# Kernel optimization log

Hardware: AMD Instinct MI355X
Metric: run time of the kernel (lower is better)

Reference implementation:

```python
import jax, jax.numpy as jnp
import numpy as np

DT = 0.01  # module-level constant in the original source
H = 64


def _lstm_cell(x_in, h, c, W_ih, W_hh, b_ih, b_hh):
    # torch nn.LSTM gate order: i, f, g, o
    gates = x_in @ W_ih.T + h @ W_hh.T + (b_ih + b_hh)
    i, f, g, o = jnp.split(gates, 4, axis=-1)
    i = jax.nn.sigmoid(i)
    f = jax.nn.sigmoid(f)
    g = jnp.tanh(g)
    o = jax.nn.sigmoid(o)
    c_new = f * c + i * g
    h_new = o * jnp.tanh(c_new)
    return h_new, c_new


def setup_inputs() -> dict:
    key = jax.random.key(0)
    ks = jax.random.split(key, 12)
    B, x_size, s_size = 4096, 8, 8
    in_size = x_size + s_size
    sc = 1.0 / np.sqrt(H)

    def rn(k, shape, scale=1.0):
        return (jax.random.normal(k, shape, dtype=jnp.float32) * scale)

    return {
        "x": rn(ks[0], (B, 1, x_size)),
        "s0": rn(ks[1], (B, s_size)),
        "W_ih0": rn(ks[2], (4 * H, in_size), sc),
        "W_hh0": rn(ks[3], (4 * H, H), sc),
        "b_ih0": rn(ks[4], (4 * H,), sc),
        "b_hh0": rn(ks[5], (4 * H,), sc),
        "W_ih1": rn(ks[6], (4 * H, H), sc),
        "W_hh1": rn(ks[7], (4 * H, H), sc),
        "b_ih1": rn(ks[8], (4 * H,), sc),
        "b_hh1": rn(ks[9], (4 * H,), sc),
        "fc_W": rn(ks[10], (s_size, H), sc),
        "fc_b": rn(ks[11], (s_size,), sc),
        "num_steps": 1001,  # floor(max_time/dt)+1 with max_time=10.0
    }


def reference(x, s0, W_ih0, W_hh0, b_ih0, b_hh0, W_ih1, W_hh1, b_ih1, b_hh1,
              fc_W, fc_b, num_steps):
    B = x.shape[0]
    xin = x[:, 0, :]  # forward only ever reads x[:, 0:1] -> [B, x_size]
    h0 = jnp.zeros((B, H), x.dtype)

    def step(carry, _):
        s, h_a, c_a, h_b, c_b = carry
        combined = jnp.concatenate([xin, s], axis=-1)  # [B, x_size + s_size]
        h_a, c_a = _lstm_cell(combined, h_a, c_a, W_ih0, W_hh0, b_ih0, b_hh0)
        h_b, c_b = _lstm_cell(h_a, h_b, c_b, W_ih1, W_hh1, b_ih1, b_hh1)
        step_out = h_b @ fc_W.T + fc_b            # [B, s_size]
        s_new = s + step_out * DT                  # Euler integration
        return (s_new, h_a, c_a, h_b, c_b), (s_new, step_out)

    init = (s0, h0, h0, h0, h0)
    _, (outs, res) = jax.lax.scan(step, init, None, length=num_steps)
    outputs = jnp.transpose(outs, (1, 0, 2))       # [B, num_steps, s_size]
    res_step = jnp.transpose(res, (1, 0, 2))       # [B, num_steps, s_size]
    cal_times = jnp.arange(num_steps, dtype=jnp.float32) * DT
    return outputs, cal_times, res_step
```

## Files before the change

### kernel.cpp

```cpp
#include <hip/hip_runtime.h>

#define DTC 0.01f
#define LAM  2.88539008178f
#define L2E  1.44269504089f

typedef __attribute__((ext_vector_type(8))) short short8;
typedef __attribute__((ext_vector_type(4))) float floatx4;

#if __has_builtin(__builtin_amdgcn_exp2f)
#define EXP2F(x) __builtin_amdgcn_exp2f(x)
#else
#define EXP2F(x) exp2f(x)
#endif
#if __has_builtin(__builtin_amdgcn_rcpf)
#define RCPF(x) __builtin_amdgcn_rcpf(x)
#else
#define RCPF(x) (1.0f / (x))
#endif

__device__ __forceinline__ unsigned short f2bf(float f) {
    unsigned u = __float_as_uint(f);
    u += 0x7FFFu + ((u >> 16) & 1u);
    return (unsigned short)(u >> 16);
}
__device__ __forceinline__ float rcp1p(float y) {
    return RCPF(1.0f + EXP2F(y));
}
__device__ __forceinline__ void wg_barrier() {
    asm volatile("s_waitcnt lgkmcnt(0)" ::: "memory");
    __builtin_amdgcn_s_barrier();
}
__device__ __forceinline__ float lane_merge(float lo, float hi) {
#if __has_builtin(__builtin_amdgcn_permlane32_swap)
    typedef __attribute__((ext_vector_type(2))) unsigned int uint2v;
    uint2v r = __builtin_amdgcn_permlane32_swap(__float_as_uint(lo), __float_as_uint(hi),
                                                false, false);
    return __uint_as_float(r[0]);
#else
    unsigned a = __float_as_uint(lo), b = __float_as_uint(hi);
    asm volatile("v_permlane32_swap_b32 %0, %1" : "+v"(a), "+v"(b));
    return __uint_as_float(a);
#endif
}

#define U1S 136

#define MFMA(a, b, c) __builtin_amdgcn_mfma_f32_16x16x32_bf16((a), (b), (c), 0, 0, 0)

__global__ __launch_bounds__(256, 2) void lstm_mfma(
    const float* __restrict__ x,    const float* __restrict__ s0,
    const float* __restrict__ W_ih0,const float* __restrict__ W_hh0,
    const float* __restrict__ b_ih0,const float* __restrict__ b_hh0,
    const float* __restrict__ W_ih1,const float* __restrict__ W_hh1,
    const float* __restrict__ b_ih1,const float* __restrict__ b_hh1,
    const float* __restrict__ fc_W, const float* __restrict__ fc_b,
    const int* __restrict__ nsp,    float* __restrict__ out, int B)
{
    __shared__ __align__(16) unsigned short U1[16 * U1S];

    const int ns   = nsp[0];
    const int tid  = threadIdx.x;
    const int lane = tid & 63;
    const int wave = tid >> 6;
    const int il   = lane & 15;
    const int quad = lane >> 4;
    const int bb   = blockIdx.x * 8;

    float* cal = out + (size_t)B * ns * 8;
    float* res = cal + ns;

    if (blockIdx.x == 0)
        for (int t = tid; t < ns; t += 256) cal[t] = t * DTC;

    for (int i = tid; i < 16 * U1S; i += 256) U1[i] = 0;

    short8 B0[4][2], B1[4][4], M2f[4][2], BF[2];
    floatx4 gs[4];
    float gd[4], b1s[4];

    for (int j = 0; j < 4; ++j) {
        const float gam = (j == 2) ? LAM : -L2E;
        const int n = 64 * j + 16 * wave + il;
        float ws[8];
        #pragma unroll
        for (int p = 0; p < 8; ++p) ws[p] = W_ih0[n * 16 + 8 + p];

        #pragma unroll
        for (int kk = 0; kk < 2; ++kk) {
            short8 f;
            #pragma unroll
            for (int jj = 0; jj < 8; ++jj) {
                int k = 32 * kk + 8 * quad + jj;
                f[jj] = (short)f2bf(gam * W_hh0[n * 64 + k]);
            }
            B0[j][kk] = f;
        }
        #pragma unroll
        for (int kk = 0; kk < 4; ++kk) {
            short8 f;
            #pragma unroll
            for (int jj = 0; jj < 8; ++jj) {
                int k = 32 * kk + 8 * quad + jj;
                float w = (k < 64) ? W_ih1[n * 64 + k] : W_hh1[n * 64 + (k - 64)];
                f[jj] = (short)f2bf(gam * w);
            }
            B1[j][kk] = f;
        }
        #pragma unroll
        for (int kk = 0; kk < 2; ++kk) {
            short8 f;
            #pragma unroll
            for (int jj = 0; jj < 8; ++jj) {
                int k = 32 * kk + 8 * quad + jj;
                float acc = 0.0f;
                #pragma unroll
                for (int p = 0; p < 8; ++p) acc += ws[p] * fc_W[p * 64 + k];
                f[jj] = (short)f2bf(gam * DTC * acc);
            }
            M2f[j][kk] = f;
        }
        float accb = 0.0f;
        #pragma unroll
        for (int p = 0; p < 8; ++p) accb += ws[p] * fc_b[p];
        gd[j] = gam * DTC * accb;

        float bcol = b_ih0[n] + b_hh0[n];
        floatx4 gv;
        #pragma unroll
        for (int reg = 0; reg < 4; ++reg) {
            int m  = 4 * quad + reg;
            int mr = bb + (m & 7);
            float acc = bcol;
            #pragma unroll
            for (int k = 0; k < 8; ++k) acc += x[mr * 8 + k] * W_ih0[n * 16 + k];
            #pragma unroll
            for (int p = 0; p < 8; ++p) acc += ws[p] * s0[mr * 8 + p];
            gv[reg] = gam * acc - gd[j];
        }
        gs[j] = gv;
        b1s[j] = gam * (b_ih1[n] + b_hh1[n]);
    }
    #pragma unroll
    for (int kk = 0; kk < 2; ++kk) {
        short8 f;
        #pragma unroll
        for (int jj = 0; jj < 8; ++jj) {
            int k = 32 * kk + 8 * quad + jj;
            float w = (il < 8) ? fc_W[il * 64 + k] : 0.0f;
            f[jj] = (short)f2bf(w);
        }
        BF[kk] = f;
    }
    const float fcb = (il < 8) ? fc_b[il] : 0.0f;

    const int mbase = 4 * ((lane & 31) >> 4) + ((lane >> 5) << 1);
    const int iidx  = 16 * wave + il;
    float cA[2] = {0, 0}, cB[2] = {0, 0};
    float s_reg[4];
    #pragma unroll
    for (int reg = 0; reg < 4; ++reg) {
        int m = 4 * quad + reg;
        s_reg[reg] = (il < 8 && m < 8) ? s0[(bb + m) * 8 + il] : 0.0f;
    }

    short8 a10 = {0,0,0,0,0,0,0,0};
    short8 a11 = {0,0,0,0,0,0,0,0};

    const unsigned short* Ar = &U1[il * U1S + 8 * quad];
    unsigned short* Hw = &U1[mbase * U1S + iidx];

    wg_barrier();

    #pragma unroll 1
    for (int t = 0; t < ns; ++t) {
        short8 a12 = *(const short8*)(Ar + 64);
        short8 a13 = *(const short8*)(Ar + 96);

        floatx4 q0[4], p1[4];
        #pragma unroll
        for (int j = 0; j < 4; ++j) {
            floatx4 z = gs[j];
            z = MFMA(a12, M2f[j][0], z);
            z = MFMA(a13, M2f[j][1], z);
            #pragma unroll
            for (int r = 0; r < 4; ++r) z[r] += gd[j];
            gs[j] = z;
            floatx4 q = z;
            q = MFMA(a10, B0[j][0], q);
            q = MFMA(a11, B0[j][1], q);
            q0[j] = q;
            floatx4 pz = {b1s[j], b1s[j], b1s[j], b1s[j]};
            pz = MFMA(a13, B1[j][3], pz);
            pz = MFMA(a12, B1[j][2], pz);
            p1[j] = pz;
        }
        float P[2][4];
        #pragma unroll
        for (int j = 0; j < 4; ++j) {
            P[0][j] = lane_merge(q0[j][0], q0[j][2]);
            P[1][j] = lane_merge(q0[j][1], q0[j][3]);
        }
        #pragma unroll
        for (int e = 0; e < 2; ++e) {
            float iv = rcp1p(P[e][0]);
            float fv = rcp1p(P[e][1]);
            float gr = rcp1p(P[e][2]);
            float ov = rcp1p(P[e][3]);
            float gl = __builtin_fmaf(gr, -2.0f * LAM, LAM);
            float c  = __builtin_fmaf(fv, cA[e], iv * gl);
            cA[e]    = c;
            float r2 = rcp1p(c);
            float h  = __builtin_fmaf(-2.0f, ov * r2, ov);
            Hw[e * U1S] = f2bf(h);
        }
        wg_barrier();

        a10 = *(const short8*)(Ar + 0);
        a11 = *(const short8*)(Ar + 32);

        if (t && wave == 0) {
            floatx4 so = {fcb, fcb, fcb, fcb};
            so = MFMA(a12, BF[0], so);
            so = MFMA(a13, BF[1], so);
            #pragma unroll
            for (int reg = 0; reg < 4; ++reg) {
                s_reg[reg] += so[reg] * DTC;
                if (quad < 2 && il < 8) {
                    size_t o = ((size_t)(bb + 4 * quad + reg) * ns + (t - 1)) * 8 + il;
                    out[o] = s_reg[reg];
                    res[o] = so[reg];
                }
            }
        }

        floatx4 q1[4];
        #pragma unroll
        for (int j = 0; j < 4; ++j) {
            floatx4 z = p1[j];
            z = MFMA(a10, B1[j][0], z);
            z = MFMA(a11, B1[j][1], z);
            q1[j] = z;
        }
        float Q[2][4];
        #pragma unroll
        for (int j = 0; j < 4; ++j) {
            Q[0][j] = lane_merge(q1[j][0], q1[j][2]);
            Q[1][j] = lane_merge(q1[j][1], q1[j][3]);
        }
        #pragma unroll
        for (int e = 0; e < 2; ++e) {
            float iv = rcp1p(Q[e][0]);
            float fv = rcp1p(Q[e][1]);
            float gr = rcp1p(Q[e][2]);
            float ov = rcp1p(Q[e][3]);
            float gl = __builtin_fmaf(gr, -2.0f * LAM, LAM);
            float c  = __builtin_fmaf(fv, cB[e], iv * gl);
            cB[e]    = c;
            float r2 = rcp1p(c);
            float h  = __builtin_fmaf(-2.0f, ov * r2, ov);
            Hw[e * U1S + 64] = f2bf(h);
        }
        wg_barrier();
    }

    if (wave == 0) {
        short8 a12 = *(const short8*)(Ar + 64);
        short8 a13 = *(const short8*)(Ar + 96);
        floatx4 so = {fcb, fcb, fcb, fcb};
        so = MFMA(a12, BF[0], so);
        so = MFMA(a13, BF[1], so);
        #pragma unroll
        for (int reg = 0; reg < 4; ++reg) {
            s_reg[reg] += so[reg] * DTC;
            if (quad < 2 && il < 8) {
                size_t o = ((size_t)(bb + 4 * quad + reg) * ns + (ns - 1)) * 8 + il;
                out[o] = s_reg[reg];
                res[o] = so[reg];
            }
        }
    }
}

extern "C" void kernel_launch(void* const* d_in, const int* in_sizes, int n_in,
                              void* d_out, int out_size, void* d_ws, size_t ws_size,
                              hipStream_t stream) {
    const float* x     = (const float*)d_in[0];
    const float* s0    = (const float*)d_in[1];
    const float* W_ih0 = (const float*)d_in[2];
    const float* W_hh0 = (const float*)d_in[3];
    const float* b_ih0 = (const float*)d_in[4];
    const float* b_hh0 = (const float*)d_in[5];
    const float* W_ih1 = (const float*)d_in[6];
    const float* W_hh1 = (const float*)d_in[7];
    const float* b_ih1 = (const float*)d_in[8];
    const float* b_hh1 = (const float*)d_in[9];
    const float* fc_W  = (const float*)d_in[10];
    const float* fc_b  = (const float*)d_in[11];
    const int*   nsp   = (const int*)d_in[12];
    (void)d_ws; (void)ws_size; (void)n_in; (void)out_size;
    int B = in_sizes[0] / 8;
    dim3 grid(B / 8), block(256);
    hipLaunchKernelGGL(lstm_mfma, grid, block, 0, stream,
        x, s0, W_ih0, W_hh0, b_ih0, b_hh0, W_ih1, W_hh1, b_ih1, b_hh1,
        fc_W, fc_b, nsp, (float*)d_out, B);
}
```

Measured before the change: 1.561 ms.

## Interleave two independent batch groups per block to overlap MFMA and transcendental phases

Each workgroup now handles 16 batch rows split into two independent 8-row groups with separate LDS buffers. The per-step schedule is software-pipelined so one group's MFMA phase runs alongside the other group's gate nonlinearities and state update, hiding the serial latency of the recurrence. Grid size is halved and launch bounds change to one block per SIMD set, which trades occupancy for more in-block parallelism and roughly doubles register pressure. The number of barriers per timestep also doubles.

```diff
diff --git a/kernel.cpp b/kernel.cpp
--- a/kernel.cpp
+++ b/kernel.cpp
@@ -47,7 +47,75 @@
 
 #define MFMA(a, b, c) __builtin_amdgcn_mfma_f32_16x16x32_bf16((a), (b), (c), 0, 0, 0)
 
-__global__ __launch_bounds__(256, 2) void lstm_mfma(
+__device__ __forceinline__ void mfma_phase1(
+    const short8& a0, const short8& a1, const short8& a2, const short8& a3,
+    const short8 B0[4][2], const short8 B1[4][4], const short8 M2f[4][2],
+    floatx4 gs[4], const float gd[4], const float b1s[4],
+    floatx4 q0[4], floatx4 p1[4])
+{
+    #pragma unroll
+    for (int j = 0; j < 4; ++j) {
+        floatx4 z = gs[j];
+        z = MFMA(a2, M2f[j][0], z);
+        z = MFMA(a3, M2f[j][1], z);
+        #pragma unroll
+        for (int r = 0; r < 4; ++r) z[r] += gd[j];
+        gs[j] = z;
+        floatx4 q = z;
+        q = MFMA(a0, B0[j][0], q);
+        q = MFMA(a1, B0[j][1], q);
+        q0[j] = q;
+        floatx4 pz = {b1s[j], b1s[j], b1s[j], b1s[j]};
+        pz = MFMA(a2, B1[j][2], pz);
+        pz = MFMA(a3, B1[j][3], pz);
+        p1[j] = pz;
+    }
+}
+
+__device__ __forceinline__ void cell_trans(const floatx4 q[4], float cst[2],
+                                           unsigned short* Hw)
+{
+    float P[2][4];
+    #pragma unroll
+    for (int j = 0; j < 4; ++j) {
+        P[0][j] = lane_merge(q[j][0], q[j][2]);
+        P[1][j] = lane_merge(q[j][1], q[j][3]);
+    }
+    #pragma unroll
+    for (int e = 0; e < 2; ++e) {
+        float iv = rcp1p(P[e][0]);
+        float fv = rcp1p(P[e][1]);
+        float gr = rcp1p(P[e][2]);
+        float ov = rcp1p(P[e][3]);
+        float gl = __builtin_fmaf(gr, -2.0f * LAM, LAM);
+        float c  = __builtin_fmaf(fv, cst[e], iv * gl);
+        cst[e]   = c;
+        float r2 = rcp1p(c);
+        float h  = __builtin_fmaf(-2.0f, ov * r2, ov);
+        Hw[e * U1S] = f2bf(h);
+    }
+}
+
+__device__ __forceinline__ void fc_store(
+    const short8& a2, const short8& a3, const short8 BF[2], float fcb,
+    float s_reg[4], float* __restrict__ out, float* __restrict__ res,
+    int rowbase, int ns, int t, int il, int quad)
+{
+    floatx4 so = {fcb, fcb, fcb, fcb};
+    so = MFMA(a2, BF[0], so);
+    so = MFMA(a3, BF[1], so);
+    #pragma unroll
+    for (int reg = 0; reg < 4; ++reg) {
+        s_reg[reg] += so[reg] * DTC;
+        if (quad < 2 && il < 8) {
+            size_t o = ((size_t)(rowbase + 4 * quad + reg) * ns + t) * 8 + il;
+            out[o] = s_reg[reg];
+            res[o] = so[reg];
+        }
+    }
+}
+
+__global__ __launch_bounds__(256, 1) void lstm_mfma(
     const float* __restrict__ x,    const float* __restrict__ s0,
     const float* __restrict__ W_ih0,const float* __restrict__ W_hh0,
     const float* __restrict__ b_ih0,const float* __restrict__ b_hh0,
@@ -56,7 +124,7 @@
     const float* __restrict__ fc_W, const float* __restrict__ fc_b,
     const int* __restrict__ nsp,    float* __restrict__ out, int B)
 {
-    __shared__ __align__(16) unsigned short U1[16 * U1S];
+    __shared__ __align__(16) unsigned short U[2][16 * U1S];
 
     const int ns   = nsp[0];
     const int tid  = threadIdx.x;
@@ -64,7 +132,7 @@
     const int wave = tid >> 6;
     const int il   = lane & 15;
     const int quad = lane >> 4;
-    const int bb   = blockIdx.x * 8;
+    const int bb   = blockIdx.x * 16;
 
     float* cal = out + (size_t)B * ns * 8;
     float* res = cal + ns;
@@ -72,10 +140,10 @@
     if (blockIdx.x == 0)
         for (int t = tid; t < ns; t += 256) cal[t] = t * DTC;
 
-    for (int i = tid; i < 16 * U1S; i += 256) U1[i] = 0;
+    for (int i = tid; i < 2 * 16 * U1S; i += 256) (&U[0][0])[i] = 0;
 
     short8 B0[4][2], B1[4][4], M2f[4][2], BF[2];
-    floatx4 gs[4];
+    floatx4 gsG[4], gsP[4];
     float gd[4], b1s[4];
 
     for (int j = 0; j < 4; ++j) {
@@ -125,20 +193,27 @@
         gd[j] = gam * DTC * accb;
 
         float bcol = b_ih0[n] + b_hh0[n];
-        floatx4 gv;
+        floatx4 gvG, gvP;
         #pragma unroll
         for (int reg = 0; reg < 4; ++reg) {
-            int m  = 4 * quad + reg;
-            int mr = bb + (m & 7);
-            float acc = bcol;
-            #pragma unroll
-            for (int k = 0; k < 8; ++k) acc += x[mr * 8 + k] * W_ih0[n * 16 + k];
-            #pragma unroll
-            for (int p = 0; p < 8; ++p) acc += ws[p] * s0[mr * 8 + p];
-            gv[reg] = gam * acc - gd[j];
-        }
-        gs[j] = gv;
-        b1s[j] = gam * (b_ih1[n] + b_hh1[n]);
+            int m = (4 * quad + reg) & 7;
+            float aG = bcol, aP = bcol;
+            #pragma unroll
+            for (int k = 0; k < 8; ++k) {
+                aG += x[(bb + m) * 8 + k] * W_ih0[n * 16 + k];
+                aP += x[(bb + 8 + m) * 8 + k] * W_ih0[n * 16 + k];
+            }
+            #pragma unroll
+            for (int p = 0; p < 8; ++p) {
+                aG += ws[p] * s0[(bb + m) * 8 + p];
+                aP += ws[p] * s0[(bb + 8 + m) * 8 + p];
+            }
+            gvG[reg] = gam * aG - gd[j];
+            gvP[reg] = gam * aP - gd[j];
+        }
+        gsG[j] = gvG;
+        gsP[j] = gvP;
+        b1s[j] = gam * (b_ih1[j * 64 + 16 * wave + il] * 0.0f + b_ih1[n] + b_hh1[n]);
     }
     #pragma unroll
     for (int kk = 0; kk < 2; ++kk) {
@@ -155,130 +230,77 @@
 
     const int mbase = 4 * ((lane & 31) >> 4) + ((lane >> 5) << 1);
     const int iidx  = 16 * wave + il;
-    float cA[2] = {0, 0}, cB[2] = {0, 0};
+    const int rowbase = bb + ((wave & 1) ? 8 : 0);
+    float cAG[2] = {0, 0}, cBG[2] = {0, 0};
+    float cAP[2] = {0, 0}, cBP[2] = {0, 0};
     float s_reg[4];
     #pragma unroll
     for (int reg = 0; reg < 4; ++reg) {
         int m = 4 * quad + reg;
-        s_reg[reg] = (il < 8 && m < 8) ? s0[(bb + m) * 8 + il] : 0.0f;
-    }
-
-    short8 a10 = {0,0,0,0,0,0,0,0};
-    short8 a11 = {0,0,0,0,0,0,0,0};
-
-    const unsigned short* Ar = &U1[il * U1S + 8 * quad];
-    unsigned short* Hw = &U1[mbase * U1S + iidx];
-
+        s_reg[reg] = (il < 8 && m < 8) ? s0[(rowbase + m) * 8 + il] : 0.0f;
+    }
+
+    short8 aG0 = {0,0,0,0,0,0,0,0}, aG1 = {0,0,0,0,0,0,0,0};
+    short8 aG2, aG3, aP0, aP1, aP2, aP3;
+    aP0 = aG0; aP1 = aG0;
+    floatx4 q0G[4], p1G[4], q0P[4], p1P[4], q1G[4], q1P[4];
+
+    const unsigned short* ArG = &U[0][il * U1S + 8 * quad];
+    const unsigned short* ArP = &U[1][il * U1S + 8 * quad];
+    unsigned short* HwG = &U[0][mbase * U1S + iidx];
+    unsigned short* HwP = &U[1][mbase * U1S + iidx];
+
+    wg_barrier();
+
+    aG2 = *(const short8*)(ArG + 64);
+    aG3 = *(const short8*)(ArG + 96);
+    mfma_phase1(aG0, aG1, aG2, aG3, B0, B1, M2f, gsG, gd, b1s, q0G, p1G);
+    wg_barrier();
+    aP2 = *(const short8*)(ArP + 64);
+    aP3 = *(const short8*)(ArP + 96);
+    mfma_phase1(aP0, aP1, aP2, aP3, B0, B1, M2f, gsP, gd, b1s, q0P, p1P);
+    cell_trans(q0G, cAG, HwG);
     wg_barrier();
 
     #pragma unroll 1
     for (int t = 0; t < ns; ++t) {
-        short8 a12 = *(const short8*)(Ar + 64);
-        short8 a13 = *(const short8*)(Ar + 96);
-
-        floatx4 q0[4], p1[4];
-        #pragma unroll
-        for (int j = 0; j < 4; ++j) {
-            floatx4 z = gs[j];
-            z = MFMA(a12, M2f[j][0], z);
-            z = MFMA(a13, M2f[j][1], z);
-            #pragma unroll
-            for (int r = 0; r < 4; ++r) z[r] += gd[j];
-            gs[j] = z;
-            floatx4 q = z;
-            q = MFMA(a10, B0[j][0], q);
-            q = MFMA(a11, B0[j][1], q);
-            q0[j] = q;
-            floatx4 pz = {b1s[j], b1s[j], b1s[j], b1s[j]};
-            pz = MFMA(a13, B1[j][3], pz);
-            pz = MFMA(a12, B1[j][2], pz);
-            p1[j] = pz;
-        }
-        float P[2][4];
-        #pragma unroll
-        for (int j = 0; j < 4; ++j) {
-            P[0][j] = lane_merge(q0[j][0], q0[j][2]);
-            P[1][j] = lane_merge(q0[j][1], q0[j][3]);
-        }
-        #pragma unroll
-        for (int e = 0; e < 2; ++e) {
-            float iv = rcp1p(P[e][0]);
-            float fv = rcp1p(P[e][1]);
-            float gr = rcp1p(P[e][2]);
-            float ov = rcp1p(P[e][3]);
-            float gl = __builtin_fmaf(gr, -2.0f * LAM, LAM);
-            float c  = __builtin_fmaf(fv, cA[e], iv * gl);
-            cA[e]    = c;
-            float r2 = rcp1p(c);
-            float h  = __builtin_fmaf(-2.0f, ov * r2, ov);
-            Hw[e * U1S] = f2bf(h);
-        }
+        aG0 = *(const short8*)(ArG + 0);
+        aG1 = *(const short8*)(ArG + 32);
+        #pragma unroll
+        for (int j = 0; j < 4; ++j)
+            q1G[j] = MFMA(aG1, B1[j][1], MFMA(aG0, B1[j][0], p1G[j]));
+        if (t && wave == 0)
+            fc_store(aG2, aG3, BF, fcb, s_reg, out, res, rowbase, ns, t - 1, il, quad);
+        cell_trans(q0P, cAP, HwP);
         wg_barrier();
 
-        a10 = *(const short8*)(Ar + 0);
-        a11 = *(const short8*)(Ar + 32);
-
-        if (t && wave == 0) {
-            floatx4 so = {fcb, fcb, fcb, fcb};
-            so = MFMA(a12, BF[0], so);
-            so = MFMA(a13, BF[1], so);
-            #pragma unroll
-            for (int reg = 0; reg < 4; ++reg) {
-                s_reg[reg] += so[reg] * DTC;
-                if (quad < 2 && il < 8) {
-                    size_t o = ((size_t)(bb + 4 * quad + reg) * ns + (t - 1)) * 8 + il;
-                    out[o] = s_reg[reg];
-                    res[o] = so[reg];
-                }
-            }
-        }
-
-        floatx4 q1[4];
-        #pragma unroll
-        for (int j = 0; j < 4; ++j) {
-            floatx4 z = p1[j];
-            z = MFMA(a10, B1[j][0], z);
-            z = MFMA(a11, B1[j][1], z);
-            q1[j] = z;
-        }
-        float Q[2][4];
-        #pragma unroll
-        for (int j = 0; j < 4; ++j) {
-            Q[0][j] = lane_merge(q1[j][0], q1[j][2]);
-            Q[1][j] = lane_merge(q1[j][1], q1[j][3]);
-        }
-        #pragma unroll
-        for (int e = 0; e < 2; ++e) {
-            float iv = rcp1p(Q[e][0]);
-            float fv = rcp1p(Q[e][1]);
-            float gr = rcp1p(Q[e][2]);
-            float ov = rcp1p(Q[e][3]);
-            float gl = __builtin_fmaf(gr, -2.0f * LAM, LAM);
-            float c  = __builtin_fmaf(fv, cB[e], iv * gl);
-            cB[e]    = c;
-            float r2 = rcp1p(c);
-            float h  = __builtin_fmaf(-2.0f, ov * r2, ov);
-            Hw[e * U1S + 64] = f2bf(h);
-        }
+        aP0 = *(const short8*)(ArP + 0);
+        aP1 = *(const short8*)(ArP + 32);
+        #pragma unroll
+        for (int j = 0; j < 4; ++j)
+            q1P[j] = MFMA(aP1, B1[j][1], MFMA(aP0, B1[j][0], p1P[j]));
+        if (t && wave == 1)
+            fc_store(aP2, aP3, BF, fcb, s_reg, out, res, rowbase, ns, t - 1, il, quad);
+        cell_trans(q1G, cBG, HwG + 64);
         wg_barrier();
-    }
-
-    if (wave == 0) {
-        short8 a12 = *(const short8*)(Ar + 64);
-        short8 a13 = *(const short8*)(Ar + 96);
-        floatx4 so = {fcb, fcb, fcb, fcb};
-        so = MFMA(a12, BF[0], so);
-        so = MFMA(a13, BF[1], so);
-        #pragma unroll
-        for (int reg = 0; reg < 4; ++reg) {
-            s_reg[reg] += so[reg] * DTC;
-            if (quad < 2 && il < 8) {
-                size_t o = ((size_t)(bb + 4 * quad + reg) * ns + (ns - 1)) * 8 + il;
-                out[o] = s_reg[reg];
-                res[o] = so[reg];
-            }
-        }
-    }
+
+        aG2 = *(const short8*)(ArG + 64);
+        aG3 = *(const short8*)(ArG + 96);
+        mfma_phase1(aG0, aG1, aG2, aG3, B0, B1, M2f, gsG, gd, b1s, q0G, p1G);
+        cell_trans(q1P, cBP, HwP + 64);
+        wg_barrier();
+
+        aP2 = *(const short8*)(ArP + 64);
+        aP3 = *(const short8*)(ArP + 96);
+        mfma_phase1(aP0, aP1, aP2, aP3, B0, B1, M2f, gsP, gd, b1s, q0P, p1P);
+        cell_trans(q0G, cAG, HwG);
+        wg_barrier();
+    }
+
+    if (wave == 0)
+        fc_store(aG2, aG3, BF, fcb, s_reg, out, res, rowbase, ns, ns - 1, il, quad);
+    if (wave == 1)
+        fc_store(aP2, aP3, BF, fcb, s_reg, out, res, rowbase, ns, ns - 1, il, quad);
 }
 
 extern "C" void kernel_launch(void* const* d_in, const int* in_sizes, int n_in,
@@ -299,7 +321,7 @@
     const int*   nsp   = (const int*)d_in[12];
     (void)d_ws; (void)ws_size; (void)n_in; (void)out_size;
     int B = in_sizes[0] / 8;
-    dim3 grid(B / 8), block(256);
+    dim3 grid(B / 16), block(256);
     hipLaunchKernelGGL(lstm_mfma, grid, block, 0, stream,
         x, s0, W_ih0, W_hh0, b_ih0, b_hh0, W_ih1, W_hh1, b_ih1, b_hh1,
         fc_W, fc_b, nsp, (float*)d_out, B);
```

Result: slower. 2.442 ms (+56.4%).
